# Kernel optimization log

Measured on AMD Instinct MI355X. Metric: run time of the kernel, lower is better.

## Reference

```python
import jax, jax.numpy as jnp
import numpy as np

B, H, S, DK = 2, 16, 2048, 64


def setup_inputs() -> dict:
    key = jax.random.key(0)
    k1, k2, k3, k4 = jax.random.split(key, 4)
    Q = jax.random.normal(k1, (B, H, S, DK), dtype=jnp.float32)
    K = jax.random.normal(k2, (B, H, S, DK), dtype=jnp.float32)
    V = jax.random.normal(k3, (B, H, S, DK), dtype=jnp.float32)
    attn_mask = jax.random.randint(k4, (B, 1, S, S), 0, 2).astype(jnp.bool_)
    return {"Q": Q, "K": K, "V": V, "attn_mask": attn_mask}


def reference(Q, K, V, attn_mask):
    d_k = Q.shape[-1]
    scale = 1.0 / jnp.sqrt(jnp.asarray(d_k, dtype=Q.dtype))
    # scores: [B,H,S,S]
    scores = jnp.einsum('bhqd,bhkd->bhqk', Q, K) * scale
    scores = jnp.where(attn_mask, jnp.asarray(-1e9, dtype=scores.dtype), scores)
    attn = jax.nn.softmax(scores, axis=-1)
    # dropout in eval mode (identity) for deterministic reference
    return jnp.einsum('bhqk,bhkd->bhqd', attn, V)
```

## Files before the change

### kernel.cpp

```cpp
#include <hip/hip_runtime.h>
#include <hip/hip_bf16.h>

#define Bdim 2
#define Hdim 16
#define Sdim 2048
#define Ddim 64
#define KVBLK 64
#define NT (Sdim / KVBLK)
#define WQ 32
#define NWAVE 4
#define QTILE (WQ * NWAVE)
#define QSCL (0.125f * 1.44269504088896f)
#define SCALE 0.125f
#define BUFE 8192
#define VOFF 4096

typedef __bf16 bf16x8 __attribute__((ext_vector_type(8)));
typedef float  f32x4  __attribute__((ext_vector_type(4)));
typedef float  f32x16 __attribute__((ext_vector_type(16)));
typedef unsigned u32x4 __attribute__((ext_vector_type(4)));

__device__ __forceinline__ void gll16(const __bf16* g, __bf16* l) {
  __builtin_amdgcn_global_load_lds(
      (const __attribute__((address_space(1))) void*)g,
      (__attribute__((address_space(3))) void*)l, 16, 0, 0);
}
__device__ __forceinline__ unsigned cvtpk_raw(float lo, float hi) {
  unsigned r;
  asm("v_cvt_pk_bf16_f32 %0, %1, %2" : "=v"(r) : "v"(lo), "v"(hi));
  return r;
}
template <bool SW>
__device__ __forceinline__ unsigned pko(float a, float b) {
  return SW ? cvtpk_raw(b, a) : cvtpk_raw(a, b);
}
__device__ __forceinline__ unsigned cvtpk(float a, float b, bool sw) {
  const float lo = sw ? b : a;
  const float hi = sw ? a : b;
  return cvtpk_raw(lo, hi);
}
template <bool SW>
__device__ __forceinline__ void packAll(const float (&sv0)[16],
                                        const float (&sv1)[16],
                                        unsigned (&pw)[16]) {
#pragma unroll
  for (int ks = 0; ks < 4; ++ks) {
    const int rb = 8 * (ks & 1);
    if (ks < 2) {
      pw[ks * 4 + 0] = pko<SW>(sv0[rb + 0], sv0[rb + 1]);
      pw[ks * 4 + 1] = pko<SW>(sv0[rb + 2], sv0[rb + 3]);
      pw[ks * 4 + 2] = pko<SW>(sv0[rb + 4], sv0[rb + 5]);
      pw[ks * 4 + 3] = pko<SW>(sv0[rb + 6], sv0[rb + 7]);
    } else {
      pw[ks * 4 + 0] = pko<SW>(sv1[rb + 0], sv1[rb + 1]);
      pw[ks * 4 + 1] = pko<SW>(sv1[rb + 2], sv1[rb + 3]);
      pw[ks * 4 + 2] = pko<SW>(sv1[rb + 4], sv1[rb + 5]);
      pw[ks * 4 + 3] = pko<SW>(sv1[rb + 6], sv1[rb + 7]);
    }
  }
}

__device__ __forceinline__ void pswap(unsigned& a, unsigned& b) {
  asm volatile("v_permlane32_swap_b32 %0, %1" : "+v"(a), "+v"(b));
}
template <bool SEMA>
__device__ __forceinline__ void exchAll(unsigned (&pw)[16], bf16x8 (&pb)[4]) {
#pragma unroll
  for (int ks = 0; ks < 4; ++ks) {
    unsigned W0 = pw[ks * 4 + 0], W1 = pw[ks * 4 + 1];
    unsigned X0 = pw[ks * 4 + 2], X1 = pw[ks * 4 + 3];
    if (SEMA) {
      pswap(W0, X0);
      pswap(W1, X1);
    } else {
      pswap(X0, W0);
      pswap(X1, W1);
    }
    u32x4 wv;
    wv[0] = W0; wv[1] = W1; wv[2] = X0; wv[3] = X1;
    pb[ks] = __builtin_bit_cast(bf16x8, wv);
  }
}

__global__ __launch_bounds__(256) void prep_all(
    const void* __restrict__ mask, unsigned long long* __restrict__ packed,
    const float* __restrict__ K, const float* __restrict__ V,
    __bf16* __restrict__ Kb, __bf16* __restrict__ Vt) {
  __shared__ __bf16 tile[64][72];
  const int t = threadIdx.x;

  if (blockIdx.x < 512) {
    const int nwords = Bdim * Sdim * (Sdim / 64);
    const unsigned* m32 = (const unsigned*)mask;
    const unsigned char* m8 = (const unsigned char*)mask;
    int gid = blockIdx.x * 256 + t;
    int lane = gid & 63;
    int wid = gid >> 6;
    const int nwaves = 512 * 256 / 64;
    bool isBytes = __any(m32[lane] > 1u);
    for (int w = wid; w < nwords; w += nwaves) {
      int v = isBytes ? (int)m8[(size_t)w * 64 + lane]
                      : (int)m32[(size_t)w * 64 + lane];
      unsigned long long bal = __ballot(v != 0);
      if (lane == 0) packed[w] = bal;
    }
    return;
  }

  const int idx = blockIdx.x - 512;
  const int bh = idx >> 5, st = idx & 31;
  const int r = t >> 2, c0 = (t & 3) << 4;
  {
    const float* ks = K + ((size_t)bh * Sdim + st * 64 + r) * Ddim + c0;
    bf16x8 o0, o1;
#pragma unroll
    for (int j = 0; j < 8; ++j) o0[j] = (__bf16)ks[j];
#pragma unroll
    for (int j = 0; j < 8; ++j) o1[j] = (__bf16)ks[8 + j];
    __bf16* kd = Kb + ((size_t)bh * Sdim + st * 64 + r) * Ddim + c0;
    *(bf16x8*)kd = o0;
    *(bf16x8*)(kd + 8) = o1;
  }
  {
    const float* vs = V + ((size_t)bh * Sdim + st * 64 + r) * Ddim + c0;
#pragma unroll
    for (int j = 0; j < 16; ++j) tile[r][c0 + j] = (__bf16)vs[j];
  }
  __syncthreads();
  {
    const int d = t >> 2, s0 = (t & 3) << 4;
    __bf16 o[16];
#pragma unroll
    for (int j = 0; j < 16; ++j) o[j] = tile[s0 + j][d];
    __bf16* dst = Vt + ((size_t)bh * Ddim + d) * Sdim + st * 64 + s0;
    *(bf16x8*)dst = *(bf16x8*)&o[0];
    *(bf16x8*)(dst + 8) = *(bf16x8*)&o[8];
  }
}

__global__ __launch_bounds__(256, 2) void attn4(
    const float* __restrict__ Q, const __bf16* __restrict__ Kb,
    const __bf16* __restrict__ Vt,
    const unsigned long long* __restrict__ maskP, float* __restrict__ Out) {
  __shared__ alignas(16) __bf16 sm[3 * BUFE];

  const int tid = threadIdx.x;
  const int lane = tid & 63;
  const int w = tid >> 6;
  const int l31 = lane & 31;
  const int hi = lane >> 5;
  const int rsw = l31 & 7;

  const int bid = blockIdx.x;
  const int bh = bid & 31;
  const int qt = bid >> 5;
  const int b = bh >> 4;
  const int qrow = qt * QTILE + w * WQ + l31;

  const __bf16* Kbase = Kb + (size_t)bh * Sdim * Ddim;
  const __bf16* Vbase = Vt + (size_t)bh * (size_t)Ddim * Sdim;
  const unsigned long long* mp =
      maskP + ((size_t)b * Sdim + qrow) * (Sdim / 64);

  const bool sw = (cvtpk_raw(0.0f, 1.0f) & 0xFFFFu) != 0u;

  bool semA;
  {
    unsigned p0 = hi ? 222u : 111u;
    unsigned p1 = hi ? 444u : 333u;
    pswap(p0, p1);
    semA = __any(hi && (p0 == 333u));
  }

  bf16x8 qf[4];
  {
    const float* qs = Q + ((size_t)bh * Sdim + qrow) * Ddim;
#pragma unroll
    for (int step = 0; step < 4; ++step) {
      const int d0 = step * 16 + hi * 8;
      float4 a = *(const float4*)(qs + d0);
      float4 c = *(const float4*)(qs + d0 + 4);
      u32x4 f;
      f[0] = cvtpk(a.x * QSCL, a.y * QSCL, sw);
      f[1] = cvtpk(a.z * QSCL, a.w * QSCL, sw);
      f[2] = cvtpk(c.x * QSCL, c.y * QSCL, sw);
      f[3] = cvtpk(c.z * QSCL, c.w * QSCL, sw);
      qf[step] = __builtin_bit_cast(bf16x8, f);
    }
  }

  const int srow = 16 * w + (lane >> 3);
  const int sblk = (lane & 7) ^ ((lane >> 3) & 7);
  const int dstw = w * 1024;

#define STAGE(off_, kt_)                                                        \
  do {                                                                          \
    const __bf16* kp_ = Kbase + ((size_t)(kt_)*KVBLK + srow) * Ddim + sblk * 8; \
    gll16(kp_, &sm[(off_) + dstw]);                                             \
    gll16(kp_ + 8 * Ddim, &sm[(off_) + dstw + 512]);                            \
    const __bf16* vp_ =                                                         \
        Vbase + (size_t)srow * Sdim + (size_t)(kt_)*KVBLK + sblk * 8;           \
    gll16(vp_, &sm[(off_) + VOFF + dstw]);                                      \
    gll16(vp_ + 8 * Sdim, &sm[(off_) + VOFF + dstw + 512]);                     \
  } while (0)

  f32x16 otA = {0,0,0,0,0,0,0,0,0,0,0,0,0,0,0,0};
  f32x16 otB = {0,0,0,0,0,0,0,0,0,0,0,0,0,0,0,0};
  float lrow = 0.f;

  unsigned long long mwCur = mp[0];
  STAGE(0, 0);
  int rdOff = 0, stOff = BUFE;

#pragma unroll 1
  for (int kt = 0; kt < NT; ++kt) {
    const unsigned long long mwNext = mp[kt + 1 < NT ? kt + 1 : NT - 1];
    if (kt + 1 < NT) {
      STAGE(stOff, kt + 1);
      asm volatile("s_waitcnt vmcnt(5)" ::: "memory");
    } else {
      asm volatile("s_waitcnt vmcnt(1)" ::: "memory");
    }
    __builtin_amdgcn_s_barrier();
    __builtin_amdgcn_sched_barrier(0);

    f32x16 st0 = {0,0,0,0,0,0,0,0,0,0,0,0,0,0,0,0};
    f32x16 st1 = {0,0,0,0,0,0,0,0,0,0,0,0,0,0,0,0};
    __builtin_amdgcn_s_setprio(1);
#pragma unroll
    for (int step = 0; step < 4; ++step) {
      bf16x8 kf = *(const bf16x8*)&sm[rdOff + l31 * 64 + (((step * 2 + hi) ^ rsw) << 3)];
      st0 = __builtin_amdgcn_mfma_f32_32x32x16_bf16(kf, qf[step], st0, 0, 0, 0);
    }
#pragma unroll
    for (int step = 0; step < 4; ++step) {
      bf16x8 kf = *(const bf16x8*)&sm[rdOff + (32 + l31) * 64 + (((step * 2 + hi) ^ rsw) << 3)];
      st1 = __builtin_amdgcn_mfma_f32_32x32x16_bf16(kf, qf[step], st1, 0, 0, 0);
    }
    __builtin_amdgcn_s_setprio(0);

    float sv0[16], sv1[16];
    const unsigned nw0s = (~(unsigned)mwCur) >> (hi * 4);
    const unsigned nw1s = (~(unsigned)(mwCur >> 32)) >> (hi * 4);
#pragma unroll
    for (int r = 0; r < 16; ++r) {
      const int cr = (r & 3) + 8 * (r >> 2);
      const float e0 = __builtin_amdgcn_exp2f(st0[r]);
      const float e1 = __builtin_amdgcn_exp2f(st1[r]);
      const int k0 = ((int)(nw0s << (31 - cr))) >> 31;
      const int k1 = ((int)(nw1s << (31 - cr))) >> 31;
      sv0[r] = __builtin_bit_cast(float, __builtin_bit_cast(int, e0) & k0);
      sv1[r] = __builtin_bit_cast(float, __builtin_bit_cast(int, e1) & k1);
    }

    float s8[8];
#pragma unroll
    for (int j = 0; j < 8; ++j)
      s8[j] = (sv0[j] + sv0[j + 8]) + (sv1[j] + sv1[j + 8]);
    lrow += ((s8[0] + s8[4]) + (s8[1] + s8[5])) +
            ((s8[2] + s8[6]) + (s8[3] + s8[7]));

    unsigned pw[16];
    if (!sw) packAll<false>(sv0, sv1, pw);
    else     packAll<true>(sv0, sv1, pw);
    bf16x8 pb[4];
    if (semA) exchAll<true>(pw, pb);
    else      exchAll<false>(pw, pb);

    __builtin_amdgcn_s_setprio(1);
#pragma unroll
    for (int ks = 0; ks < 4; ++ks) {
      bf16x8 vf = *(const bf16x8*)&sm[rdOff + VOFF + l31 * 64 + (((ks * 2 + hi) ^ rsw) << 3)];
      otA = __builtin_amdgcn_mfma_f32_32x32x16_bf16(vf, pb[ks], otA, 0, 0, 0);
    }
#pragma unroll
    for (int ks = 0; ks < 4; ++ks) {
      bf16x8 vf = *(const bf16x8*)&sm[rdOff + VOFF + (32 + l31) * 64 + (((ks * 2 + hi) ^ rsw) << 3)];
      otB = __builtin_amdgcn_mfma_f32_32x32x16_bf16(vf, pb[ks], otB, 0, 0, 0);
    }
    __builtin_amdgcn_s_setprio(0);

    mwCur = mwNext;
    rdOff = stOff;
    stOff = (stOff == 2 * BUFE) ? 0 : stOff + BUFE;
  }
#undef STAGE

  lrow += __shfl_xor(lrow, 32, 64);
  const float inv = 1.f / (lrow + 1e-30f);
  float* orow = Out + ((size_t)bh * Sdim + qrow) * Ddim;
#pragma unroll
  for (int g = 0; g < 4; ++g) {
    const int d0 = 8 * g + 4 * hi;
    float4 va = {otA[4 * g] * inv, otA[4 * g + 1] * inv,
                 otA[4 * g + 2] * inv, otA[4 * g + 3] * inv};
    float4 vb = {otB[4 * g] * inv, otB[4 * g + 1] * inv,
                 otB[4 * g + 2] * inv, otB[4 * g + 3] * inv};
    *(float4*)(orow + d0) = va;
    *(float4*)(orow + 32 + d0) = vb;
  }
}

__global__ __launch_bounds__(256) void attn_fallback(
    const float* __restrict__ Q, const float* __restrict__ K,
    const float* __restrict__ V, const void* __restrict__ maskRaw,
    float* __restrict__ Out) {
  __shared__ alignas(16) __bf16 Kl[KVBLK * Ddim];
  __shared__ alignas(16) __bf16 Vts[Ddim * KVBLK];
  __shared__ alignas(16) __bf16 Pl[4][16 * 64];

  const int tid = threadIdx.x;
  const int lane = tid & 63;
  const int w = tid >> 6;
  const int lhi = lane >> 4;
  const int llo = lane & 15;

  const int qt = blockIdx.x;
  const int bh = blockIdx.y;
  const int b = bh >> 4;
  const int qbase = qt * 64;

  const float* Qp = Q + (size_t)bh * Sdim * Ddim;
  const float* Kp = K + (size_t)bh * Sdim * Ddim;
  const float* Vp = V + (size_t)bh * Sdim * Ddim;

  bool maskBytes = __any(((const unsigned*)maskRaw)[lane] > 1u);

  bf16x8 qf0, qf1;
  {
    const int qr = qbase + w * 16 + llo;
    const float* src = Qp + (size_t)qr * Ddim + lhi * 8;
#pragma unroll
    for (int i = 0; i < 8; ++i) qf0[i] = (__bf16)(src[i] * SCALE);
#pragma unroll
    for (int i = 0; i < 8; ++i) qf1[i] = (__bf16)(src[32 + i] * SCALE);
  }

  f32x4 acc[4] = {{0.f,0.f,0.f,0.f},{0.f,0.f,0.f,0.f},
                  {0.f,0.f,0.f,0.f},{0.f,0.f,0.f,0.f}};
  float mrow[4], lrw[4];
#pragma unroll
  for (int r = 0; r < 4; ++r) { mrow[r] = -3.0e38f; lrw[r] = 0.f; }

  for (int kt = 0; kt < NT; ++kt) {
    __syncthreads();
    {
      int r = tid >> 2;
      int c0 = (tid & 3) << 4;
      const float* ks = Kp + (size_t)(kt * KVBLK + r) * Ddim + c0;
      const float* vs = Vp + (size_t)(kt * KVBLK + r) * Ddim + c0;
      float kv[16], vv[16];
#pragma unroll
      for (int j = 0; j < 4; ++j) {
        *(float4*)(&kv[j * 4]) = *(const float4*)(ks + j * 4);
        *(float4*)(&vv[j * 4]) = *(const float4*)(vs + j * 4);
      }
      const int swzK = (r & 7) << 3;
      bf16x8 k0v, k1v;
#pragma unroll
      for (int j = 0; j < 8; ++j) { k0v[j] = (__bf16)kv[j]; k1v[j] = (__bf16)kv[8 + j]; }
      *(bf16x8*)&Kl[r * 64 + (c0 ^ swzK)] = k0v;
      *(bf16x8*)&Kl[r * 64 + ((c0 + 8) ^ swzK)] = k1v;
#pragma unroll
      for (int j = 0; j < 16; ++j) {
        int d = c0 + j;
        Vts[d * 64 + (r ^ ((d & 7) << 3))] = (__bf16)vv[j];
      }
    }
    __syncthreads();

    float sv[4][4];
#pragma unroll
    for (int cb = 0; cb < 4; ++cb) {
      int krow = cb * 16 + llo;
      int swz = (krow & 7) << 3;
      bf16x8 kf0 = *(const bf16x8*)&Kl[krow * 64 + ((lhi * 8) ^ swz)];
      bf16x8 kf1 = *(const bf16x8*)&Kl[krow * 64 + ((32 + lhi * 8) ^ swz)];
      f32x4 s = {0.f, 0.f, 0.f, 0.f};
      s = __builtin_amdgcn_mfma_f32_16x16x32_bf16(qf0, kf0, s, 0, 0, 0);
      s = __builtin_amdgcn_mfma_f32_16x16x32_bf16(qf1, kf1, s, 0, 0, 0);
#pragma unroll
      for (int r = 0; r < 4; ++r) {
        size_t q = qbase + w * 16 + lhi * 4 + r;
        size_t k = (size_t)kt * KVBLK + cb * 16 + llo;
        size_t idx = ((size_t)b * Sdim + q) * Sdim + k;
        bool masked = maskBytes ? (((const unsigned char*)maskRaw)[idx] != 0)
                                : (((const int*)maskRaw)[idx] != 0);
        sv[cb][r] = masked ? -1e9f : s[r];
      }
    }

    float corr[4], tsum[4];
#pragma unroll
    for (int r = 0; r < 4; ++r) {
      float mx = fmaxf(fmaxf(sv[0][r], sv[1][r]), fmaxf(sv[2][r], sv[3][r]));
#pragma unroll
      for (int off = 1; off < 16; off <<= 1)
        mx = fmaxf(mx, __shfl_xor(mx, off, 64));
      float mnew = fmaxf(mrow[r], mx);
      corr[r] = __expf(mrow[r] - mnew);
      mrow[r] = mnew;
      tsum[r] = 0.f;
    }
#pragma unroll
    for (int cb = 0; cb < 4; ++cb) {
#pragma unroll
      for (int r = 0; r < 4; ++r) {
        float p = __expf(sv[cb][r] - mrow[r]);
        tsum[r] += p;
        int row = lhi * 4 + r;
        int col = cb * 16 + llo;
        Pl[w][row * 64 + (col ^ ((row & 7) << 3))] = (__bf16)p;
      }
    }
#pragma unroll
    for (int r = 0; r < 4; ++r) {
      float s = tsum[r];
#pragma unroll
      for (int off = 1; off < 16; off <<= 1)
        s += __shfl_xor(s, off, 64);
      lrw[r] = lrw[r] * corr[r] + s;
#pragma unroll
      for (int db = 0; db < 4; ++db) acc[db][r] *= corr[r];
    }
    asm volatile("s_waitcnt lgkmcnt(0)" ::: "memory");

    bf16x8 pf0 = *(const bf16x8*)&Pl[w][llo * 64 + ((lhi * 8) ^ ((llo & 7) << 3))];
    bf16x8 pf1 = *(const bf16x8*)&Pl[w][llo * 64 + ((32 + lhi * 8) ^ ((llo & 7) << 3))];
#pragma unroll
    for (int db = 0; db < 4; ++db) {
      int d = db * 16 + llo;
      int swz = (d & 7) << 3;
      bf16x8 vf0 = *(const bf16x8*)&Vts[d * 64 + ((lhi * 8) ^ swz)];
      bf16x8 vf1 = *(const bf16x8*)&Vts[d * 64 + ((32 + lhi * 8) ^ swz)];
      acc[db] = __builtin_amdgcn_mfma_f32_16x16x32_bf16(pf0, vf0, acc[db], 0, 0, 0);
      acc[db] = __builtin_amdgcn_mfma_f32_16x16x32_bf16(pf1, vf1, acc[db], 0, 0, 0);
    }
  }

#pragma unroll
  for (int r = 0; r < 4; ++r) {
    float inv = 1.f / lrw[r];
    int q = qbase + w * 16 + lhi * 4 + r;
    float* dst = Out + ((size_t)bh * Sdim + q) * Ddim + llo;
#pragma unroll
    for (int db = 0; db < 4; ++db) dst[db * 16] = acc[db][r] * inv;
  }
}

extern "C" void kernel_launch(void* const* d_in, const int* in_sizes, int n_in,
                              void* d_out, int out_size, void* d_ws, size_t ws_size,
                              hipStream_t stream) {
  const float* Q = (const float*)d_in[0];
  const float* K = (const float*)d_in[1];
  const float* V = (const float*)d_in[2];
  const void* mask = d_in[3];
  float* out = (float*)d_out;

  const size_t packed_bytes =
      (size_t)Bdim * Sdim * (Sdim / 64) * sizeof(unsigned long long);
  const size_t tensor_bf16 = (size_t)Bdim * Hdim * Sdim * Ddim * 2;

  if (ws_size >= packed_bytes + 2 * tensor_bf16) {
    unsigned long long* packed = (unsigned long long*)d_ws;
    __bf16* Kb = (__bf16*)((char*)d_ws + packed_bytes);
    __bf16* Vt = (__bf16*)((char*)d_ws + packed_bytes + tensor_bf16);
    prep_all<<<512 + Bdim * Hdim * (Sdim / 64), 256, 0, stream>>>(
        mask, packed, K, V, Kb, Vt);
    attn4<<<(Sdim / QTILE) * Bdim * Hdim, 256, 0, stream>>>(Q, Kb, Vt, packed, out);
  } else {
    attn_fallback<<<dim3(Sdim / 64, Bdim * Hdim), 256, 0, stream>>>(Q, K, V, mask, out);
  }
}
```

Baseline: 97.27 us.

## Software-pipeline QK^T of next tile with softmax and PV of previous tile

Restructures the main loop so each iteration computes QK^T scores for the current KV tile while running the exp/mask/pack and PV MFMAs for the previous tile, with a prologue and epilogue. The LDS ring buffer grows from three to four stages so the previous tile's V stays resident while the next tile is staged. The goal is to overlap MFMA work with the VALU-heavy softmax so matrix units stay busy. In exchange it holds an extra score accumulator pair in registers and doubles-plus LDS use, which may hurt occupancy at two blocks per CU.

```diff
diff --git a/kernel.cpp b/kernel.cpp
--- a/kernel.cpp
+++ b/kernel.cpp
@@ -138,11 +138,11 @@
   }
 }
 
-__global__ __launch_bounds__(256, 2) void attn4(
+__global__ __launch_bounds__(256, 2) void attn9(
     const float* __restrict__ Q, const __bf16* __restrict__ Kb,
     const __bf16* __restrict__ Vt,
     const unsigned long long* __restrict__ maskP, float* __restrict__ Out) {
-  __shared__ alignas(16) __bf16 sm[3 * BUFE];
+  __shared__ alignas(16) __bf16 sm[4 * BUFE];
 
   const int tid = threadIdx.x;
   const int lane = tid & 63;
@@ -204,86 +204,113 @@
     gll16(vp_ + 8 * Sdim, &sm[(off_) + VOFF + dstw + 512]);                     \
   } while (0)
 
+#define QKT(OFF, d0, d1)                                                       \
+  do {                                                                         \
+    __builtin_amdgcn_s_setprio(1);                                             \
+    _Pragma("unroll") for (int step = 0; step < 4; ++step) {                   \
+      bf16x8 kf = *(const bf16x8*)&sm[(OFF) + l31 * 64 +                       \
+                                      (((step * 2 + hi) ^ rsw) << 3)];         \
+      d0 = __builtin_amdgcn_mfma_f32_32x32x16_bf16(kf, qf[step], d0, 0, 0, 0); \
+    }                                                                          \
+    _Pragma("unroll") for (int step = 0; step < 4; ++step) {                   \
+      bf16x8 kf = *(const bf16x8*)&sm[(OFF) + (32 + l31) * 64 +                \
+                                      (((step * 2 + hi) ^ rsw) << 3)];         \
+      d1 = __builtin_amdgcn_mfma_f32_32x32x16_bf16(kf, qf[step], d1, 0, 0, 0); \
+    }                                                                          \
+    __builtin_amdgcn_s_setprio(0);                                             \
+  } while (0)
+
+#define SMPV(s0, s1, MW, VOFFS)                                                \
+  do {                                                                         \
+    float sv0[16], sv1[16];                                                    \
+    const unsigned nw0s = (~(unsigned)(MW)) >> (hi * 4);                       \
+    const unsigned nw1s = (~(unsigned)((MW) >> 32)) >> (hi * 4);               \
+    _Pragma("unroll") for (int r = 0; r < 16; ++r) {                           \
+      const int cr = (r & 3) + 8 * (r >> 2);                                   \
+      const float e0 = __builtin_amdgcn_exp2f(s0[r]);                          \
+      const float e1 = __builtin_amdgcn_exp2f(s1[r]);                          \
+      const int k0 = ((int)(nw0s << (31 - cr))) >> 31;                         \
+      const int k1 = ((int)(nw1s << (31 - cr))) >> 31;                         \
+      sv0[r] = __builtin_bit_cast(float, __builtin_bit_cast(int, e0) & k0);    \
+      sv1[r] = __builtin_bit_cast(float, __builtin_bit_cast(int, e1) & k1);    \
+    }                                                                          \
+    float s8[8];                                                               \
+    _Pragma("unroll") for (int j = 0; j < 8; ++j)                              \
+      s8[j] = (sv0[j] + sv0[j + 8]) + (sv1[j] + sv1[j + 8]);                   \
+    lrow += ((s8[0] + s8[4]) + (s8[1] + s8[5])) +                              \
+            ((s8[2] + s8[6]) + (s8[3] + s8[7]));                               \
+    unsigned pw[16];                                                           \
+    if (!sw) packAll<false>(sv0, sv1, pw);                                     \
+    else     packAll<true>(sv0, sv1, pw);                                      \
+    bf16x8 pb[4];                                                              \
+    if (semA) exchAll<true>(pw, pb);                                           \
+    else      exchAll<false>(pw, pb);                                          \
+    __builtin_amdgcn_s_setprio(1);                                             \
+    _Pragma("unroll") for (int ks = 0; ks < 4; ++ks) {                         \
+      bf16x8 vf = *(const bf16x8*)&sm[(VOFFS) + VOFF + l31 * 64 +              \
+                                      (((ks * 2 + hi) ^ rsw) << 3)];           \
+      otA = __builtin_amdgcn_mfma_f32_32x32x16_bf16(vf, pb[ks], otA, 0, 0, 0); \
+    }                                                                          \
+    _Pragma("unroll") for (int ks = 0; ks < 4; ++ks) {                         \
+      bf16x8 vf = *(const bf16x8*)&sm[(VOFFS) + VOFF + (32 + l31) * 64 +       \
+                                      (((ks * 2 + hi) ^ rsw) << 3)];           \
+      otB = __builtin_amdgcn_mfma_f32_32x32x16_bf16(vf, pb[ks], otB, 0, 0, 0); \
+    }                                                                          \
+    __builtin_amdgcn_s_setprio(0);                                             \
+  } while (0)
+
   f32x16 otA = {0,0,0,0,0,0,0,0,0,0,0,0,0,0,0,0};
   f32x16 otB = {0,0,0,0,0,0,0,0,0,0,0,0,0,0,0,0};
   float lrow = 0.f;
 
   unsigned long long mwCur = mp[0];
+  unsigned long long mwPrev, mwNext;
   STAGE(0, 0);
-  int rdOff = 0, stOff = BUFE;
+  f32x16 stP0 = {0,0,0,0,0,0,0,0,0,0,0,0,0,0,0,0};
+  f32x16 stP1 = {0,0,0,0,0,0,0,0,0,0,0,0,0,0,0,0};
+  {
+    mwNext = mp[1];
+    STAGE(BUFE, 1);
+    asm volatile("s_waitcnt vmcnt(5)" ::: "memory");
+    __builtin_amdgcn_s_barrier();
+    __builtin_amdgcn_sched_barrier(0);
+    QKT(0, stP0, stP1);
+    mwPrev = mwCur;
+    mwCur = mwNext;
+  }
+  int rdPrev = 0, rdCur = BUFE, stOff = 2 * BUFE;
 
 #pragma unroll 1
-  for (int kt = 0; kt < NT; ++kt) {
-    const unsigned long long mwNext = mp[kt + 1 < NT ? kt + 1 : NT - 1];
+  for (int kt = 1; kt < NT; ++kt) {
     if (kt + 1 < NT) {
+      mwNext = mp[kt + 1];
       STAGE(stOff, kt + 1);
       asm volatile("s_waitcnt vmcnt(5)" ::: "memory");
     } else {
-      asm volatile("s_waitcnt vmcnt(1)" ::: "memory");
+      asm volatile("s_waitcnt vmcnt(0)" ::: "memory");
     }
     __builtin_amdgcn_s_barrier();
     __builtin_amdgcn_sched_barrier(0);
 
-    f32x16 st0 = {0,0,0,0,0,0,0,0,0,0,0,0,0,0,0,0};
-    f32x16 st1 = {0,0,0,0,0,0,0,0,0,0,0,0,0,0,0,0};
-    __builtin_amdgcn_s_setprio(1);
-#pragma unroll
-    for (int step = 0; step < 4; ++step) {
-      bf16x8 kf = *(const bf16x8*)&sm[rdOff + l31 * 64 + (((step * 2 + hi) ^ rsw) << 3)];
-      st0 = __builtin_amdgcn_mfma_f32_32x32x16_bf16(kf, qf[step], st0, 0, 0, 0);
-    }
-#pragma unroll
-    for (int step = 0; step < 4; ++step) {
-      bf16x8 kf = *(const bf16x8*)&sm[rdOff + (32 + l31) * 64 + (((step * 2 + hi) ^ rsw) << 3)];
-      st1 = __builtin_amdgcn_mfma_f32_32x32x16_bf16(kf, qf[step], st1, 0, 0, 0);
-    }
-    __builtin_amdgcn_s_setprio(0);
-
-    float sv0[16], sv1[16];
-    const unsigned nw0s = (~(unsigned)mwCur) >> (hi * 4);
-    const unsigned nw1s = (~(unsigned)(mwCur >> 32)) >> (hi * 4);
-#pragma unroll
-    for (int r = 0; r < 16; ++r) {
-      const int cr = (r & 3) + 8 * (r >> 2);
-      const float e0 = __builtin_amdgcn_exp2f(st0[r]);
-      const float e1 = __builtin_amdgcn_exp2f(st1[r]);
-      const int k0 = ((int)(nw0s << (31 - cr))) >> 31;
-      const int k1 = ((int)(nw1s << (31 - cr))) >> 31;
-      sv0[r] = __builtin_bit_cast(float, __builtin_bit_cast(int, e0) & k0);
-      sv1[r] = __builtin_bit_cast(float, __builtin_bit_cast(int, e1) & k1);
-    }
-
-    float s8[8];
-#pragma unroll
-    for (int j = 0; j < 8; ++j)
-      s8[j] = (sv0[j] + sv0[j + 8]) + (sv1[j] + sv1[j + 8]);
-    lrow += ((s8[0] + s8[4]) + (s8[1] + s8[5])) +
-            ((s8[2] + s8[6]) + (s8[3] + s8[7]));
-
-    unsigned pw[16];
-    if (!sw) packAll<false>(sv0, sv1, pw);
-    else     packAll<true>(sv0, sv1, pw);
-    bf16x8 pb[4];
-    if (semA) exchAll<true>(pw, pb);
-    else      exchAll<false>(pw, pb);
-
-    __builtin_amdgcn_s_setprio(1);
-#pragma unroll
-    for (int ks = 0; ks < 4; ++ks) {
-      bf16x8 vf = *(const bf16x8*)&sm[rdOff + VOFF + l31 * 64 + (((ks * 2 + hi) ^ rsw) << 3)];
-      otA = __builtin_amdgcn_mfma_f32_32x32x16_bf16(vf, pb[ks], otA, 0, 0, 0);
-    }
-#pragma unroll
-    for (int ks = 0; ks < 4; ++ks) {
-      bf16x8 vf = *(const bf16x8*)&sm[rdOff + VOFF + (32 + l31) * 64 + (((ks * 2 + hi) ^ rsw) << 3)];
-      otB = __builtin_amdgcn_mfma_f32_32x32x16_bf16(vf, pb[ks], otB, 0, 0, 0);
-    }
-    __builtin_amdgcn_s_setprio(0);
-
+    f32x16 stC0 = {0,0,0,0,0,0,0,0,0,0,0,0,0,0,0,0};
+    f32x16 stC1 = {0,0,0,0,0,0,0,0,0,0,0,0,0,0,0,0};
+    QKT(rdCur, stC0, stC1);
+
+    SMPV(stP0, stP1, mwPrev, rdPrev);
+
+    stP0 = stC0;
+    stP1 = stC1;
+    mwPrev = mwCur;
     mwCur = mwNext;
-    rdOff = stOff;
-    stOff = (stOff == 2 * BUFE) ? 0 : stOff + BUFE;
-  }
+    rdPrev = rdCur;
+    rdCur = stOff;
+    stOff = (stOff == 3 * BUFE) ? 0 : stOff + BUFE;
+  }
+
+  SMPV(stP0, stP1, mwPrev, rdPrev);
+
+#undef SMPV
+#undef QKT
 #undef STAGE
 
   lrow += __shfl_xor(lrow, 32, 64);
@@ -467,7 +494,7 @@
     __bf16* Vt = (__bf16*)((char*)d_ws + packed_bytes + tensor_bf16);
     prep_all<<<512 + Bdim * Hdim * (Sdim / 64), 256, 0, stream>>>(
         mask, packed, K, V, Kb, Vt);
-    attn4<<<(Sdim / QTILE) * Bdim * Hdim, 256, 0, stream>>>(Q, Kb, Vt, packed, out);
+    attn9<<<(Sdim / QTILE) * Bdim * Hdim, 256, 0, stream>>>(Q, Kb, Vt, packed, out);
   } else {
     attn_fallback<<<dim3(Sdim / 64, Bdim * Hdim), 256, 0, stream>>>(Q, K, V, mask, out);
   }
```

After: 97.25 us. About the same (-0.0%).
